# Performance work log

Measured on AMD Instinct MI355X. Metric: run time of the kernel, lower is better.

## Reference

```python
import jax, jax.numpy as jnp
import numpy as np

NUM_HEADS = 16


def setup_inputs() -> dict:
    key = jax.random.key(0)
    ks = jax.random.split(key, 8)
    B, N, C = 2, 1024, 1024
    H, D = NUM_HEADS, C // NUM_HEADS
    Npast = 8192
    s = 0.02
    return {
        "x": jax.random.normal(ks[0], (B, N, C), jnp.float32),
        "past_k": jax.random.normal(ks[1], (B, H, Npast, D), jnp.float32),
        "past_v": jax.random.normal(ks[2], (B, H, Npast, D), jnp.float32),
        "qkv_w": jax.random.normal(ks[3], (3 * C, C), jnp.float32) * s,
        "qkv_b": jax.random.normal(ks[4], (3 * C,), jnp.float32) * s,
        "proj_w": jax.random.normal(ks[5], (C, C), jnp.float32) * s,
        "proj_b": jax.random.normal(ks[6], (C,), jnp.float32) * s,
        "cache_budget": 4096,
    }


def reference(x, past_k, past_v, qkv_w, qkv_b, proj_w, proj_b, cache_budget):
    B, N, C = x.shape
    H = NUM_HEADS
    D = C // H
    scale = D ** -0.5

    # fused QKV projection -> [3, B, H, N, D]
    qkv = (x @ qkv_w.T + qkv_b).reshape(B, N, 3, H, D).transpose(2, 0, 3, 1, 4)
    q, k, v = qkv[0], qkv[1], qkv[2]

    # use_cache path: anchor tokens = current-frame token count on first call
    num_anchor = N
    k = jnp.concatenate([past_k, k], axis=2)  # [B,H,Ntot,D]
    v = jnp.concatenate([past_v, v], axis=2)
    Ntot = k.shape[2]

    # eviction: mean cosine-similarity scoring over candidate (non-anchor) keys.
    # mean_j cos(k_i, k_j) == khat_i . mean_j(khat_j) -- O(N*D), no NxN matrix.
    num_keep = cache_budget - num_anchor
    cand_k = k[:, :, num_anchor:, :]  # [B,H,Ncand,D]
    khat = cand_k / (jnp.linalg.norm(cand_k, axis=-1, keepdims=True) + 1e-6)
    mean_dir = khat.mean(axis=2, keepdims=True)
    mean_scores = (khat * mean_dir).sum(-1)  # [B,H,Ncand]
    # keep the least-redundant tokens (lowest mean similarity)
    _, top_idx = jax.lax.top_k(-mean_scores, num_keep)  # [B,H,num_keep]
    top_idx = jnp.sort(top_idx, axis=-1)
    avg_scores = mean_scores.mean()

    anchor_idx = jnp.broadcast_to(jnp.arange(num_anchor)[None, None, :], (B, H, num_anchor))
    keep_idx = jnp.concatenate([anchor_idx, top_idx + num_anchor], axis=2)  # [B,H,budget]
    gidx = keep_idx[..., None]
    k_new = jnp.take_along_axis(k, jnp.broadcast_to(gidx, (B, H, cache_budget, D)), axis=2)
    v_new = jnp.take_along_axis(v, jnp.broadcast_to(gidx, (B, H, cache_budget, D)), axis=2)

    # SDPA
    logits = jnp.einsum("bhqd,bhkd->bhqk", q, k_new) * scale
    attn = jax.nn.softmax(logits, axis=-1)
    o = jnp.einsum("bhqk,bhkd->bhqd", attn, v_new)
    o = o.transpose(0, 2, 1, 3).reshape(B, N, C)
    out = o @ proj_w.T + proj_b
    return out, k_new, v_new, avg_scores
```

## Files before the change

### kernel.cpp

```cpp
#include <hip/hip_runtime.h>
#include <hip/hip_bf16.h>
#include <math.h>

#define BB 2
#define HH 16
#define NN 1024
#define CC 1024
#define DD 64
#define NPAST 8192
#define NANCH 1024
#define CBUD 4096
#define NKEEP 3072
#define NCAND 8192
#define BH 32

#define TILEB 16384

#define OUT_SZ   (BB*NN*CC)
#define KNEW_OFF ((size_t)OUT_SZ)
#define KNEW_SZ  ((size_t)BH*CBUD*DD)
#define VNEW_OFF (KNEW_OFF + KNEW_SZ)
#define AVG_OFF  (VNEW_OFF + KNEW_SZ)

#define WS_KF   ((size_t)0)
#define WS_VF   ((size_t)2097152)
#define WS_VTS  ((size_t)0)
#define WS_XT   ((size_t)4194304)
#define WS_OT   ((size_t)4194304)
#define WS_WQVT ((size_t)5242880)
#define WS_WPT  ((size_t)5242880)
#define WS_QB   ((size_t)6291456)
#define WS_MD   ((size_t)7340032)
#define WS_SC   ((size_t)7342080)
#define WS_BS   ((size_t)7604224)
#define WS_SEL  ((size_t)7604288)
#define WS_MDP  ((size_t)7702592)
#define WS_BSP  ((size_t)7718976)

typedef __attribute__((ext_vector_type(8))) short short8;
typedef __attribute__((ext_vector_type(4))) float f32x4;

typedef unsigned int __attribute__((address_space(3))) lds_uint;
typedef unsigned int __attribute__((address_space(1))) glb_uint;

__device__ __forceinline__ void gload16(const void* g, void* l) {
    __builtin_amdgcn_global_load_lds((const glb_uint*)g, (lds_uint*)l, 16, 0, 0);
}

__device__ inline unsigned short f2bf(float f) {
    unsigned u = __float_as_uint(f);
    unsigned r = (u + 0x7FFFu + ((u >> 16) & 1u)) >> 16;
    return (unsigned short)r;
}
__device__ inline unsigned cvtpk(float a, float b) {
    __hip_bfloat162 h = __float22bfloat162_rn(make_float2(a, b));
    return *reinterpret_cast<unsigned*>(&h);
}
__device__ __forceinline__ float fexp2(float x) {
#if __has_builtin(__builtin_amdgcn_exp2f)
    return __builtin_amdgcn_exp2f(x);
#else
    return exp2f(x);
#endif
}

__global__ __launch_bounds__(256) void conv_xw(const float* __restrict__ x,
                                               const float* __restrict__ qw,
                                               unsigned short* __restrict__ xt,
                                               unsigned short* __restrict__ wqvt)
{
    int bid = blockIdx.x;
    int gid = (bid & 1023) * 256 + threadIdx.x;
    int r = gid >> 7, k0 = (gid & 127) * 8;
    const float* src;
    unsigned short* dst;
    int srow;
    if (bid < 1024) { src = x;  dst = xt;   srow = r; }
    else            { src = qw; dst = wqvt; srow = (r < 1024) ? r : r + 1024; }
    float4 a = *(const float4*)&src[(size_t)srow * 1024 + k0];
    float4 b = *(const float4*)&src[(size_t)srow * 1024 + k0 + 4];
    uint4 u;
    u.x = cvtpk(a.x, a.y); u.y = cvtpk(a.z, a.w);
    u.z = cvtpk(b.x, b.y); u.w = cvtpk(b.z, b.w);
    size_t tile = (size_t)(r >> 7) * 16 + (k0 >> 6);
    int inner = (((r & 127) * 128 + (k0 & 63) * 2)) ^ ((r & 7) << 4);
    *(uint4*)((char*)dst + tile * TILEB + inner) = u;
}

__global__ __launch_bounds__(256) void kf_gemm(const float* __restrict__ x,
                                               const float* __restrict__ w,
                                               const float* __restrict__ bias,
                                               float* __restrict__ ws)
{
    __shared__ float As[2][16][68];
    __shared__ float Bs[2][16][68];
    int tid = threadIdx.x;
    int m0 = blockIdx.y * 64;
    int n0 = blockIdx.x * 64;
    int tx = tid & 15, ty = tid >> 4;
    int lr = tid >> 2;
    int lk = (tid & 3) * 4;
    float acc[4][4] = {{0.f}};

    {
        float4 a = *(const float4*)&x[(size_t)(m0 + lr) * CC + lk];
        float4 b = *(const float4*)&w[(size_t)(1024 + n0 + lr) * CC + lk];
        As[0][lk+0][lr] = a.x; As[0][lk+1][lr] = a.y; As[0][lk+2][lr] = a.z; As[0][lk+3][lr] = a.w;
        Bs[0][lk+0][lr] = b.x; Bs[0][lk+1][lr] = b.y; Bs[0][lk+2][lr] = b.z; Bs[0][lk+3][lr] = b.w;
    }
    __syncthreads();

    int cur = 0;
    for (int k0 = 0; k0 < CC; k0 += 16) {
        float4 a, b;
        bool more = (k0 + 16 < CC);
        if (more) {
            a = *(const float4*)&x[(size_t)(m0 + lr) * CC + k0 + 16 + lk];
            b = *(const float4*)&w[(size_t)(1024 + n0 + lr) * CC + k0 + 16 + lk];
        }
        float tacc[4][4] = {{0.f}};
        #pragma unroll
        for (int kk = 0; kk < 16; ++kk) {
            float4 a4 = *(const float4*)&As[cur][kk][ty*4];
            float4 b4 = *(const float4*)&Bs[cur][kk][tx*4];
            float av[4] = {a4.x, a4.y, a4.z, a4.w};
            float bv[4] = {b4.x, b4.y, b4.z, b4.w};
            #pragma unroll
            for (int i = 0; i < 4; ++i)
                #pragma unroll
                for (int j = 0; j < 4; ++j)
                    tacc[i][j] += av[i] * bv[j];
        }
        #pragma unroll
        for (int i = 0; i < 4; ++i)
            #pragma unroll
            for (int j = 0; j < 4; ++j)
                acc[i][j] += tacc[i][j];
        if (more) {
            As[cur^1][lk+0][lr] = a.x; As[cur^1][lk+1][lr] = a.y;
            As[cur^1][lk+2][lr] = a.z; As[cur^1][lk+3][lr] = a.w;
            Bs[cur^1][lk+0][lr] = b.x; Bs[cur^1][lk+1][lr] = b.y;
            Bs[cur^1][lk+2][lr] = b.z; Bs[cur^1][lk+3][lr] = b.w;
        }
        __syncthreads();
        cur ^= 1;
    }

    int cn0 = n0 + tx * 4;
    int h = cn0 >> 6, dd0 = cn0 & 63;
    float4 b4 = *(const float4*)&bias[1024 + cn0];
    float* kf = ws + WS_KF;
    #pragma unroll
    for (int i = 0; i < 4; ++i) {
        int m = m0 + ty * 4 + i;
        int b2 = m >> 10, n = m & 1023;
        float4 t;
        t.x = acc[i][0] + b4.x; t.y = acc[i][1] + b4.y;
        t.z = acc[i][2] + b4.z; t.w = acc[i][3] + b4.w;
        *(float4*)&kf[(((size_t)b2*HH + h)*NN + n)*DD + dd0] = t;
    }
}

template<int MODE>
__global__ __launch_bounds__(256) void mfma_gemm(const unsigned short* __restrict__ At,
                                                 const unsigned short* __restrict__ Bt,
                                                 const float* __restrict__ bias,
                                                 float* __restrict__ outp)
{
    __shared__ char lds[131072];
    int tid = threadIdx.x;
    int w = tid >> 6, lane = tid & 63;
    int g = lane >> 4, r16 = lane & 15;
    int wr = w >> 1, wc = w & 1;
    int bm = blockIdx.y, bn = blockIdx.x;
    const int KB = 16;
    const float QSCL = 0.125f * 1.44269504089f;

    f32x4 acc[4][4];
    #pragma unroll
    for (int i = 0; i < 4; ++i)
        #pragma unroll
        for (int j = 0; j < 4; ++j) acc[i][j] = 0.f;

    const char* Abase = (const char*)At + (size_t)bm * KB * TILEB;
    const char* Bbase = (const char*)Bt + (size_t)bn * KB * TILEB;

    #pragma unroll
    for (int i = 0; i < 4; ++i) {
        gload16(Abase + (size_t)w*4096 + i*1024 + lane*16, lds + w*4096 + i*1024);
        gload16(Bbase + (size_t)w*4096 + i*1024 + lane*16, lds + TILEB + w*4096 + i*1024);
    }
    asm volatile("s_waitcnt vmcnt(0)" ::: "memory");
    __syncthreads();

    int cur = 0;
    for (int kb = 0; kb < KB; ++kb) {
        char* Acur = lds + cur * (2*TILEB);
        char* Bcur = Acur + TILEB;
        if (kb + 1 < KB) {
            char* Anxt = lds + (cur ^ 1) * (2*TILEB);
            char* Bnxt = Anxt + TILEB;
            const char* an = Abase + (size_t)(kb+1)*TILEB + w*4096;
            const char* bsrc = Bbase + (size_t)(kb+1)*TILEB + w*4096;
            #pragma unroll
            for (int i = 0; i < 4; ++i) {
                gload16(an + i*1024 + lane*16, Anxt + w*4096 + i*1024);
                gload16(bsrc + i*1024 + lane*16, Bnxt + w*4096 + i*1024);
            }
        }
        short8 a0[4], a1[4], b0[4], b1[4];
        #pragma unroll
        for (int mi = 0; mi < 4; ++mi) {
            int row = wr*64 + mi*16 + r16;
            int sw = (row & 7) << 4;
            a0[mi] = *(const short8*)(Acur + ((row*128 + g*16) ^ sw));
            a1[mi] = *(const short8*)(Acur + ((row*128 + 64 + g*16) ^ sw));
        }
        #pragma unroll
        for (int ni = 0; ni < 4; ++ni) {
            int row = wc*64 + ni*16 + r16;
            int sw = (row & 7) << 4;
            b0[ni] = *(const short8*)(Bcur + ((row*128 + g*16) ^ sw));
            b1[ni] = *(const short8*)(Bcur + ((row*128 + 64 + g*16) ^ sw));
        }
        __builtin_amdgcn_s_setprio(1);
        #pragma unroll
        for (int mi = 0; mi < 4; ++mi)
            #pragma unroll
            for (int ni = 0; ni < 4; ++ni) {
                acc[mi][ni] = __builtin_amdgcn_mfma_f32_16x16x32_bf16(a0[mi], b0[ni], acc[mi][ni], 0, 0, 0);
                acc[mi][ni] = __builtin_amdgcn_mfma_f32_16x16x32_bf16(a1[mi], b1[ni], acc[mi][ni], 0, 0, 0);
            }
        __builtin_amdgcn_s_setprio(0);
        asm volatile("s_waitcnt vmcnt(0)" ::: "memory");
        __syncthreads();
        cur ^= 1;
    }

    int nq = bn*128 + wc*64;
    float bv[4];
    #pragma unroll
    for (int ni = 0; ni < 4; ++ni) {
        int n = nq + ni*16 + r16;
        bv[ni] = (MODE == 0) ? bias[(n < 1024) ? n : (n + 1024)] : bias[n];
    }
    #pragma unroll
    for (int mi = 0; mi < 4; ++mi) {
        #pragma unroll
        for (int rr = 0; rr < 4; ++rr) {
            int ml = wr*64 + mi*16 + 4*g + rr;
            int mg = bm*128 + ml;
            int bb = mg >> 10, tok = mg & 1023;
            #pragma unroll
            for (int ni = 0; ni < 4; ++ni) {
                int n = nq + ni*16 + r16;
                float v = acc[mi][ni][rr] + bv[ni];
                if (MODE == 0) {
                    if (n < 1024) {
                        unsigned short* qb = (unsigned short*)(outp + WS_QB);
                        int hh = n >> 6, d = n & 63;
                        qb[(((size_t)bb*16 + hh)*1024 + tok)*64 + d] = f2bf(v * QSCL);
                    } else {
                        float* vf = outp + WS_VF;
                        int hh = (n - 1024) >> 6, d = n & 63;
                        vf[(((size_t)bb*16 + hh)*1024 + tok)*64 + d] = v;
                    }
                } else {
                    outp[(size_t)mg*1024 + n] = v;
                }
            }
        }
    }
}

__global__ __launch_bounds__(256) void meandir_part(const float* __restrict__ past_k,
                                                    float* __restrict__ ws)
{
    int bh = blockIdx.x, seg = blockIdx.y, tid = threadIdx.x;
    const float* kpast = past_k + (size_t)bh * NPAST * DD;
    const float* knew  = ws + WS_KF + (size_t)bh * NN * DD;
    float dir[64];
    #pragma unroll
    for (int i = 0; i < 64; ++i) dir[i] = 0.f;

    int j0 = seg * 1024;
    for (int jj = tid; jj < 1024; jj += 256) {
        int pos = NANCH + j0 + jj;
        const float* row = (pos < NPAST) ? (kpast + (size_t)pos * DD)
                                         : (knew + (size_t)(pos - NPAST) * DD);
        float v[64]; float ss = 0.f;
        #pragma unroll
        for (int g = 0; g < 16; ++g) {
            float4 t = *(const float4*)&row[g*4];
            v[4*g]=t.x; v[4*g+1]=t.y; v[4*g+2]=t.z; v[4*g+3]=t.w;
            ss += t.x*t.x + t.y*t.y + t.z*t.z + t.w*t.w;
        }
        float inv = 1.0f / (sqrtf(ss) + 1e-6f);
        #pragma unroll
        for (int i = 0; i < 64; ++i) dir[i] += v[i] * inv;
    }
    #pragma unroll
    for (int i = 0; i < 64; ++i)
        for (int off = 32; off; off >>= 1) dir[i] += __shfl_xor(dir[i], off);

    __shared__ float sdir[4][64];
    int lane = tid & 63, wid = tid >> 6;
    if (lane == 0) {
        #pragma unroll
        for (int i = 0; i < 64; ++i) sdir[wid][i] = dir[i];
    }
    __syncthreads();
    if (tid < 64) {
        float s = sdir[0][tid] + sdir[1][tid] + sdir[2][tid] + sdir[3][tid];
        ws[WS_MDP + ((size_t)bh*8 + seg)*DD + tid] = s;
    }
}

__global__ void meandir_red(float* __restrict__ ws)
{
    int bh = blockIdx.x, tid = threadIdx.x;
    float s = 0.f;
    #pragma unroll
    for (int seg = 0; seg < 8; ++seg)
        s += ws[WS_MDP + ((size_t)bh*8 + seg)*DD + tid];
    ws[WS_MD + (size_t)bh*DD + tid] = s * (1.0f / (float)NCAND);
}

__global__ __launch_bounds__(256) void scores_part(const float* __restrict__ past_k,
                                                   float* __restrict__ ws)
{
    __shared__ float md[64];
    __shared__ float sred[4];
    int bh = blockIdx.x, seg = blockIdx.y, tid = threadIdx.x;
    if (tid < 64) md[tid] = ws[WS_MD + (size_t)bh*DD + tid];
    __syncthreads();
    const float* kpast = past_k + (size_t)bh * NPAST * DD;
    const float* knew  = ws + WS_KF + (size_t)bh * NN * DD;
    float ssum = 0.f;
    int j0 = seg * 1024;
    for (int jj = tid; jj < 1024; jj += 256) {
        int j = j0 + jj;
        int pos = NANCH + j;
        const float* row = (pos < NPAST) ? (kpast + (size_t)pos * DD)
                                         : (knew + (size_t)(pos - NPAST) * DD);
        float ss = 0.f, dp = 0.f;
        #pragma unroll
        for (int g = 0; g < 16; ++g) {
            float4 t = *(const float4*)&row[g*4];
            ss += t.x*t.x + t.y*t.y + t.z*t.z + t.w*t.w;
            dp += t.x*md[4*g] + t.y*md[4*g+1] + t.z*md[4*g+2] + t.w*md[4*g+3];
        }
        float sc = dp / (sqrtf(ss) + 1e-6f);
        ws[WS_SC + (size_t)bh*NCAND + j] = sc;
        ssum += sc;
    }
    for (int off = 32; off; off >>= 1) ssum += __shfl_xor(ssum, off);
    int lane = tid & 63, wid = tid >> 6;
    if (lane == 0) sred[wid] = ssum;
    __syncthreads();
    if (tid == 0)
        ws[WS_BSP + (size_t)bh*8 + seg] = sred[0] + sred[1] + sred[2] + sred[3];
}

__global__ __launch_bounds__(1024) void topk_k(float* __restrict__ ws, int* __restrict__ sel,
                                               float* __restrict__ dout)
{
    __shared__ unsigned keys[NCAND];
    __shared__ int hist[256];
    __shared__ int red[16];
    __shared__ int red2[16];
    __shared__ float fred[16];
    __shared__ int bcast;
    __shared__ unsigned bbyte;
    int bh = blockIdx.x, tid = threadIdx.x;
    int lane = tid & 63, wid = tid >> 6;

    if (bh == 0) {
        float v = (tid < 256) ? ws[WS_BSP + tid] : 0.f;
        for (int off = 32; off; off >>= 1) v += __shfl_xor(v, off);
        if (lane == 0) fred[wid] = v;
        __syncthreads();
        if (tid == 0) {
            float s = 0.f;
            for (int i = 0; i < 16; ++i) s += fred[i];
            dout[AVG_OFF] = s * (1.0f / ((float)BH * (float)NCAND));
        }
        __syncthreads();
    }

    for (int j = tid; j < NCAND; j += 1024) {
        unsigned u = __float_as_uint(ws[WS_SC + (size_t)bh*NCAND + j]);
        u ^= (u & 0x80000000u) ? 0xFFFFFFFFu : 0x80000000u;
        keys[j] = u;
    }
    __syncthreads();

    int rem = NKEEP;
    unsigned prefix = 0;
    #pragma unroll
    for (int pass = 0; pass < 4; ++pass) {
        int shift = 24 - 8*pass;
        if (tid < 256) hist[tid] = 0;
        __syncthreads();
        unsigned himask = (pass == 0) ? 0u : (0xFFFFFFFFu << (shift + 8));
        for (int j = tid; j < NCAND; j += 1024) {
            unsigned k = keys[j];
            if ((k & himask) == prefix)
                atomicAdd(&hist[(k >> shift) & 255], 1);
        }
        __syncthreads();
        if (tid == 0) {
            int cum = 0, b = 0;
            for (; b < 255; ++b) {
                if (rem <= cum + hist[b]) break;
                cum += hist[b];
            }
            bcast = cum;
            bbyte = (unsigned)b;
        }
        __syncthreads();
        rem -= bcast;
        prefix |= (bbyte << shift);
        __syncthreads();
    }
    unsigned T = prefix;

    {
        int cnt = 0;
        for (int j = tid; j < NCAND; j += 1024) cnt += (int)(keys[j] < T);
        for (int off = 32; off; off >>= 1) cnt += __shfl_xor(cnt, off);
        if (lane == 0) red[wid] = cnt;
        __syncthreads();
        if (tid == 0) { int c = 0; for (int i = 0; i < 16; ++i) c += red[i]; bcast = c; }
        __syncthreads();
    }
    int c_less = bcast;
    int ttie = NKEEP - c_less;

    int base = tid * 8;
    unsigned kv[8]; int lcnt = 0, ecnt = 0;
    #pragma unroll
    for (int i = 0; i < 8; ++i) {
        kv[i] = keys[base + i];
        lcnt += (int)(kv[i] < T);
        ecnt += (int)(kv[i] == T);
    }
    int li = lcnt, ei = ecnt;
    for (int off = 1; off < 64; off <<= 1) {
        int tl = __shfl_up(li, off);
        int te = __shfl_up(ei, off);
        if (lane >= off) { li += tl; ei += te; }
    }
    __syncthreads();
    if (lane == 63) { red[wid] = li; red2[wid] = ei; }
    __syncthreads();
    int lb = 0, eb = 0;
    for (int w = 0; w < wid; ++w) { lb += red[w]; eb += red2[w]; }
    lb += li - lcnt; eb += ei - ecnt;
    #pragma unroll
    for (int i = 0; i < 8; ++i) {
        bool less = kv[i] < T, eq = kv[i] == T;
        if (less || (eq && eb < ttie)) {
            int pos = lb + (eb < ttie ? eb : ttie);
            sel[(size_t)bh*NKEEP + pos] = base + i;
        }
        lb += (int)less; eb += (int)eq;
    }
}

__global__ __launch_bounds__(256) void gather_k(const float* __restrict__ past_k,
                                                const float* __restrict__ past_v,
                                                const float* __restrict__ ws,
                                                const int* __restrict__ sel,
                                                float* __restrict__ dout)
{
    int gid = blockIdx.x * 256 + threadIdx.x;
    int row = gid >> 4, lane = gid & 15;
    int bh = row >> 12, r = row & 4095;
    int pos = (r < NANCH) ? r : (NANCH + sel[(size_t)bh*NKEEP + (r - NANCH)]);
    const float *kr, *vr;
    if (pos < NPAST) {
        kr = past_k + ((size_t)bh*NPAST + pos) * DD;
        vr = past_v + ((size_t)bh*NPAST + pos) * DD;
    } else {
        kr = ws + WS_KF + ((size_t)bh*NN + (pos - NPAST)) * DD;
        vr = ws + WS_VF + ((size_t)bh*NN + (pos - NPAST)) * DD;
    }
    float4 kq = *(const float4*)&kr[lane*4];
    float4 vq = *(const float4*)&vr[lane*4];
    *(float4*)&dout[KNEW_OFF + ((size_t)bh*CBUD + r)*DD + lane*4] = kq;
    *(float4*)&dout[VNEW_OFF + ((size_t)bh*CBUD + r)*DD + lane*4] = vq;
}

__global__ __launch_bounds__(256) void vtrans_conv(const float* __restrict__ dout,
                                                   unsigned short* __restrict__ vt,
                                                   const float* __restrict__ pw,
                                                   unsigned short* __restrict__ wpt)
{
    if (blockIdx.x >= 2048) {
        int gid = (blockIdx.x - 2048) * 256 + threadIdx.x;
        int r = gid >> 7, k0 = (gid & 127) * 8;
        float4 a = *(const float4*)&pw[(size_t)r * 1024 + k0];
        float4 b = *(const float4*)&pw[(size_t)r * 1024 + k0 + 4];
        uint4 u;
        u.x = cvtpk(a.x, a.y); u.y = cvtpk(a.z, a.w);
        u.z = cvtpk(b.x, b.y); u.w = cvtpk(b.z, b.w);
        size_t tile = (size_t)(r >> 7) * 16 + (k0 >> 6);
        int inner = (((r & 127) * 128 + (k0 & 63) * 2)) ^ ((r & 7) << 4);
        *(uint4*)((char*)wpt + tile * TILEB + inner) = u;
        return;
    }
    __shared__ unsigned short S[64][65];
    int bh = blockIdx.x >> 6, kt = blockIdx.x & 63;
    int c0 = kt * 64;
    int tid = threadIdx.x;
    int r = tid >> 2, c4 = (tid & 3) * 16;
    const float* src = dout + VNEW_OFF + ((size_t)bh*CBUD + c0 + r)*DD + c4;
    #pragma unroll
    for (int i = 0; i < 4; ++i) {
        float4 f = *(const float4*)&src[i*4];
        S[r][c4 + i*4 + 0] = f2bf(f.x);
        S[r][c4 + i*4 + 1] = f2bf(f.y);
        S[r][c4 + i*4 + 2] = f2bf(f.z);
        S[r][c4 + i*4 + 3] = f2bf(f.w);
    }
    __syncthreads();
    int d = r, k4 = c4;
    uint4 u0, u1;
    u0.x = (unsigned)S[k4+0][d] | ((unsigned)S[k4+1][d] << 16);
    u0.y = (unsigned)S[k4+2][d] | ((unsigned)S[k4+3][d] << 16);
    u0.z = (unsigned)S[k4+4][d] | ((unsigned)S[k4+5][d] << 16);
    u0.w = (unsigned)S[k4+6][d] | ((unsigned)S[k4+7][d] << 16);
    u1.x = (unsigned)S[k4+8][d] | ((unsigned)S[k4+9][d] << 16);
    u1.y = (unsigned)S[k4+10][d] | ((unsigned)S[k4+11][d] << 16);
    u1.z = (unsigned)S[k4+12][d] | ((unsigned)S[k4+13][d] << 16);
    u1.w = (unsigned)S[k4+14][d] | ((unsigned)S[k4+15][d] << 16);
    size_t tbase = ((size_t)bh*64 + kt) * 8192;
    int sw = (d & 7) << 4;
    *(uint4*)((char*)vt + tbase + ((d*128 + k4*2)      ^ sw)) = u0;
    *(uint4*)((char*)vt + tbase + ((d*128 + k4*2 + 16) ^ sw)) = u1;
}

__global__ __launch_bounds__(256) void attn_mfma(const unsigned short* __restrict__ qb,
                                                 const float* __restrict__ dout,
                                                 const unsigned short* __restrict__ vt,
                                                 unsigned short* __restrict__ ot)
{
    __shared__ char kls[2][2][8192];
    __shared__ char vls[2][2][8192];
    __shared__ char pls[4][2048];

    int orig = blockIdx.x;
    int bid = (orig & 7) * 64 + (orig >> 3);
    int bh = bid >> 4, qt = bid & 15;
    int b = bh >> 4, h = bh & 15;
    int tid = threadIdx.x;
    int w = tid >> 6, lane = tid & 63;
    int g = lane >> 4, r16 = lane & 15;
    int q0 = qt * 64 + w * 16;

    const unsigned short* qrow = qb + ((size_t)bh*NN + q0 + r16) * DD;
    short8 qa0 = *(const short8*)&qrow[8*g];
    short8 qa1 = *(const short8*)&qrow[32 + 8*g];

    const float* kf = dout + KNEW_OFF + (size_t)bh * CBUD * DD;
    const char* vtt = (const char*)vt + (size_t)bh * 64 * 8192;
    char* plw = pls[w];
    int psw = (r16 & 7) << 4;

    int srA = tid >> 3;
    int srB = srA + 32;
    int scb = (tid & 7) * 16;
    int d0  = scb >> 1;
    int sdA = (srA*128 + scb) ^ ((srA & 7) << 4);
    int sdB = (srB*128 + scb) ^ ((srB & 7) << 4);

    f32x4 accd[4];
    #pragma unroll
    for (int dt = 0; dt < 4; ++dt) accd[dt] = 0.f;
    float lsum = 0.f;

    {
        gload16(vtt + tid*16,               vls[0][0] + tid*16);
        gload16(vtt + 4096 + tid*16,        vls[0][0] + 4096 + tid*16);
        gload16(vtt + 8192 + tid*16,        vls[0][1] + tid*16);
        gload16(vtt + 8192 + 4096 + tid*16, vls[0][1] + 4096 + tid*16);
        #pragma unroll
        for (int hh = 0; hh < 2; ++hh) {
            const float* ksA = kf + ((size_t)hh*64 + srA) * DD + d0;
            const float* ksB = kf + ((size_t)hh*64 + srB) * DD + d0;
            float4 a0 = *(const float4*)ksA, a1 = *(const float4*)(ksA + 4);
            float4 b0 = *(const float4*)ksB, b1 = *(const float4*)(ksB + 4);
            uint4 kuA, kuB;
            kuA.x = cvtpk(a0.x,a0.y); kuA.y = cvtpk(a0.z,a0.w);
            kuA.z = cvtpk(a1.x,a1.y); kuA.w = cvtpk(a1.z,a1.w);
            kuB.x = cvtpk(b0.x,b0.y); kuB.y = cvtpk(b0.z,b0.w);
            kuB.z = cvtpk(b1.x,b1.y); kuB.w = cvtpk(b1.z,b1.w);
            *(uint4*)&kls[0][hh][sdA] = kuA;
            *(uint4*)&kls[0][hh][sdB] = kuB;
        }
    }
    __syncthreads();

    int cur = 0;
    for (int t = 0; t < 32; ++t) {
        float4 na0[2], na1[2], nb0[2], nb1[2];
        bool more = (t + 1 < 32);
        if (more) {
            int nt = 2*t + 2;
            gload16(vtt + (size_t)nt*8192 + tid*16,            vls[cur^1][0] + tid*16);
            gload16(vtt + (size_t)nt*8192 + 4096 + tid*16,     vls[cur^1][0] + 4096 + tid*16);
            gload16(vtt + (size_t)(nt+1)*8192 + tid*16,        vls[cur^1][1] + tid*16);
            gload16(vtt + (size_t)(nt+1)*8192 + 4096 + tid*16, vls[cur^1][1] + 4096 + tid*16);
            #pragma unroll
            for (int hh = 0; hh < 2; ++hh) {
                const float* ksA = kf + ((size_t)(nt+hh)*64 + srA) * DD + d0;
                const float* ksB = kf + ((size_t)(nt+hh)*64 + srB) * DD + d0;
                na0[hh] = *(const float4*)ksA; na1[hh] = *(const float4*)(ksA + 4);
                nb0[hh] = *(const float4*)ksB; nb1[hh] = *(const float4*)(ksB + 4);
            }
        }

        #pragma unroll
        for (int hh = 0; hh < 2; ++hh) {
            const char* kb = kls[cur][hh];
            f32x4 sacc[4];
            #pragma unroll
            for (int t4 = 0; t4 < 4; ++t4) sacc[t4] = 0.f;
            __builtin_amdgcn_s_setprio(1);
            #pragma unroll
            for (int t4 = 0; t4 < 4; ++t4) {
                int row = 16*t4 + r16;
                int sw = (r16 & 7) << 4;
                short8 ka0 = *(const short8*)(kb + ((row*128 + g*16) ^ sw));
                short8 ka1 = *(const short8*)(kb + ((row*128 + 64 + g*16) ^ sw));
                sacc[t4] = __builtin_amdgcn_mfma_f32_16x16x32_bf16(ka0, qa0, sacc[t4], 0, 0, 0);
                sacc[t4] = __builtin_amdgcn_mfma_f32_16x16x32_bf16(ka1, qa1, sacc[t4], 0, 0, 0);
            }
            __builtin_amdgcn_s_setprio(0);

            float p[4][4];
            float ps = 0.f;
            #pragma unroll
            for (int t4 = 0; t4 < 4; ++t4) {
                p[t4][0] = fexp2(sacc[t4][0]);
                p[t4][1] = fexp2(sacc[t4][1]);
                p[t4][2] = fexp2(sacc[t4][2]);
                p[t4][3] = fexp2(sacc[t4][3]);
                ps += (p[t4][0] + p[t4][1]) + (p[t4][2] + p[t4][3]);
            }
            lsum += ps;
            #pragma unroll
            for (int t4 = 0; t4 < 4; ++t4) {
                uint2 u;
                u.x = cvtpk(p[t4][0], p[t4][1]);
                u.y = cvtpk(p[t4][2], p[t4][3]);
                int cb = (16*t4 + 4*g) * 2;
                *(uint2*)&plw[(r16*128 + cb) ^ psw] = u;
            }

            short8 pa0 = *(const short8*)&plw[(r16*128 + 16*g)      ^ psw];
            short8 pa1 = *(const short8*)&plw[(r16*128 + 64 + 16*g) ^ psw];
            const char* vb = vls[cur][hh];
            __builtin_amdgcn_s_setprio(1);
            #pragma unroll
            for (int dt = 0; dt < 4; ++dt) {
                int row = dt*16 + r16;
                int sw = (r16 & 7) << 4;
                short8 vb0 = *(const short8*)(vb + ((row*128 + g*16) ^ sw));
                short8 vb1 = *(const short8*)(vb + ((row*128 + 64 + g*16) ^ sw));
                accd[dt] = __builtin_amdgcn_mfma_f32_16x16x32_bf16(pa0, vb0, accd[dt], 0, 0, 0);
                accd[dt] = __builtin_amdgcn_mfma_f32_16x16x32_bf16(pa1, vb1, accd[dt], 0, 0, 0);
            }
            __builtin_amdgcn_s_setprio(0);
        }

        if (more) {
            #pragma unroll
            for (int hh = 0; hh < 2; ++hh) {
                uint4 kuA, kuB;
                kuA.x = cvtpk(na0[hh].x, na0[hh].y); kuA.y = cvtpk(na0[hh].z, na0[hh].w);
                kuA.z = cvtpk(na1[hh].x, na1[hh].y); kuA.w = cvtpk(na1[hh].z, na1[hh].w);
                kuB.x = cvtpk(nb0[hh].x, nb0[hh].y); kuB.y = cvtpk(nb0[hh].z, nb0[hh].w);
                kuB.z = cvtpk(nb1[hh].x, nb1[hh].y); kuB.w = cvtpk(nb1[hh].z, nb1[hh].w);
                *(uint4*)&kls[cur^1][hh][sdA] = kuA;
                *(uint4*)&kls[cur^1][hh][sdB] = kuB;
            }
        }
        __syncthreads();
        cur ^= 1;
    }

    lsum += __shfl_xor(lsum, 16);
    lsum += __shfl_xor(lsum, 32);
    float ivl = 1.0f / lsum;
    float iq[4];
    #pragma unroll
    for (int rr = 0; rr < 4; ++rr) iq[rr] = __shfl(ivl, 20*g + rr);
    #pragma unroll
    for (int dt = 0; dt < 4; ++dt) {
        #pragma unroll
        for (int rr = 0; rr < 4; ++rr) {
            int q = q0 + 4*g + rr;
            int mrow = b*1024 + q;
            int d = dt*16 + r16;
            size_t tile = (size_t)(mrow >> 7) * 16 + h;
            int inner = ((mrow & 127)*128 + d*2) ^ ((mrow & 7) << 4);
            *(unsigned short*)((char*)ot + tile*TILEB + inner) = f2bf(accd[dt][rr] * iq[rr]);
        }
    }
}

extern "C" void kernel_launch(void* const* d_in, const int* in_sizes, int n_in,
                              void* d_out, int out_size, void* d_ws, size_t ws_size,
                              hipStream_t stream)
{
    (void)in_sizes; (void)n_in; (void)out_size; (void)ws_size;
    const float* x      = (const float*)d_in[0];
    const float* past_k = (const float*)d_in[1];
    const float* past_v = (const float*)d_in[2];
    const float* qkv_w  = (const float*)d_in[3];
    const float* qkv_b  = (const float*)d_in[4];
    const float* proj_w = (const float*)d_in[5];
    const float* proj_b = (const float*)d_in[6];
    float* out = (float*)d_out;
    float* ws  = (float*)d_ws;
    int*   sel = (int*)(ws + WS_SEL);
    unsigned short* xt   = (unsigned short*)(ws + WS_XT);
    unsigned short* wqvt = (unsigned short*)(ws + WS_WQVT);
    unsigned short* wpt  = (unsigned short*)(ws + WS_WPT);
    unsigned short* qbp  = (unsigned short*)(ws + WS_QB);
    unsigned short* vtp  = (unsigned short*)(ws + WS_VTS);
    unsigned short* otp  = (unsigned short*)(ws + WS_OT);

    conv_xw<<<2048, 256, 0, stream>>>(x, qkv_w, xt, wqvt);
    kf_gemm<<<dim3(16, 32), 256, 0, stream>>>(x, qkv_w, qkv_b, ws);
    mfma_gemm<0><<<dim3(16, 16), 256, 0, stream>>>(xt, wqvt, qkv_b, ws);
    meandir_part<<<dim3(32, 8), 256, 0, stream>>>(past_k, ws);
    meandir_red<<<32, 64, 0, stream>>>(ws);
    scores_part<<<dim3(32, 8), 256, 0, stream>>>(past_k, ws);
    topk_k<<<32, 1024, 0, stream>>>(ws, sel, out);
    gather_k<<<8192, 256, 0, stream>>>(past_k, past_v, ws, sel, out);
    vtrans_conv<<<2560, 256, 0, stream>>>(out, vtp, proj_w, wpt);
    attn_mfma<<<512, 256, 0, stream>>>(qbp, out, vtp, otp);
    mfma_gemm<1><<<dim3(8, 16), 256, 0, stream>>>(otp, wpt, proj_b, out);
}
```

Measured before the change: 283.7 us.

## Pre-convert K_new to swizzled bf16 tiles and async-load them in attention

Adds a pre-pass in vtrans_conv that converts the gathered fp32 K cache into swizzled bf16 64x64 tiles in workspace, so the attention kernel can stream K with global_load_lds like V instead of loading fp32 and converting per block. It also doubles the k-step of the fp32 K-projection GEMM and hoists the LDS offset computations in the attention loop. The K path is used only when the workspace is large enough, and costs an extra global write and read of the bf16 K tiles.

```diff
diff --git a/kernel.cpp b/kernel.cpp
--- a/kernel.cpp
+++ b/kernel.cpp
@@ -36,6 +36,7 @@
 #define WS_SEL  ((size_t)7604288)
 #define WS_MDP  ((size_t)7702592)
 #define WS_BSP  ((size_t)7718976)
+#define WS_KTS  ((size_t)7719232)
 
 typedef __attribute__((ext_vector_type(8))) short short8;
 typedef __attribute__((ext_vector_type(4))) float f32x4;
@@ -92,8 +93,8 @@
                                                const float* __restrict__ bias,
                                                float* __restrict__ ws)
 {
-    __shared__ float As[2][16][68];
-    __shared__ float Bs[2][16][68];
+    __shared__ float As[2][32][68];
+    __shared__ float Bs[2][32][68];
     int tid = threadIdx.x;
     int m0 = blockIdx.y * 64;
     int n0 = blockIdx.x * 64;
@@ -103,44 +104,57 @@
     float acc[4][4] = {{0.f}};
 
     {
-        float4 a = *(const float4*)&x[(size_t)(m0 + lr) * CC + lk];
-        float4 b = *(const float4*)&w[(size_t)(1024 + n0 + lr) * CC + lk];
-        As[0][lk+0][lr] = a.x; As[0][lk+1][lr] = a.y; As[0][lk+2][lr] = a.z; As[0][lk+3][lr] = a.w;
-        Bs[0][lk+0][lr] = b.x; Bs[0][lk+1][lr] = b.y; Bs[0][lk+2][lr] = b.z; Bs[0][lk+3][lr] = b.w;
+        float4 a0 = *(const float4*)&x[(size_t)(m0 + lr) * CC + lk];
+        float4 a1 = *(const float4*)&x[(size_t)(m0 + lr) * CC + lk + 16];
+        float4 b0 = *(const float4*)&w[(size_t)(1024 + n0 + lr) * CC + lk];
+        float4 b1 = *(const float4*)&w[(size_t)(1024 + n0 + lr) * CC + lk + 16];
+        As[0][lk+0][lr] = a0.x; As[0][lk+1][lr] = a0.y; As[0][lk+2][lr] = a0.z; As[0][lk+3][lr] = a0.w;
+        As[0][lk+16][lr] = a1.x; As[0][lk+17][lr] = a1.y; As[0][lk+18][lr] = a1.z; As[0][lk+19][lr] = a1.w;
+        Bs[0][lk+0][lr] = b0.x; Bs[0][lk+1][lr] = b0.y; Bs[0][lk+2][lr] = b0.z; Bs[0][lk+3][lr] = b0.w;
+        Bs[0][lk+16][lr] = b1.x; Bs[0][lk+17][lr] = b1.y; Bs[0][lk+18][lr] = b1.z; Bs[0][lk+19][lr] = b1.w;
     }
     __syncthreads();
 
     int cur = 0;
-    for (int k0 = 0; k0 < CC; k0 += 16) {
-        float4 a, b;
-        bool more = (k0 + 16 < CC);
+    for (int k0 = 0; k0 < CC; k0 += 32) {
+        float4 a0, a1, b0, b1;
+        bool more = (k0 + 32 < CC);
         if (more) {
-            a = *(const float4*)&x[(size_t)(m0 + lr) * CC + k0 + 16 + lk];
-            b = *(const float4*)&w[(size_t)(1024 + n0 + lr) * CC + k0 + 16 + lk];
-        }
-        float tacc[4][4] = {{0.f}};
-        #pragma unroll
-        for (int kk = 0; kk < 16; ++kk) {
-            float4 a4 = *(const float4*)&As[cur][kk][ty*4];
-            float4 b4 = *(const float4*)&Bs[cur][kk][tx*4];
-            float av[4] = {a4.x, a4.y, a4.z, a4.w};
-            float bv[4] = {b4.x, b4.y, b4.z, b4.w};
+            a0 = *(const float4*)&x[(size_t)(m0 + lr) * CC + k0 + 32 + lk];
+            a1 = *(const float4*)&x[(size_t)(m0 + lr) * CC + k0 + 48 + lk];
+            b0 = *(const float4*)&w[(size_t)(1024 + n0 + lr) * CC + k0 + 32 + lk];
+            b1 = *(const float4*)&w[(size_t)(1024 + n0 + lr) * CC + k0 + 48 + lk];
+        }
+        #pragma unroll
+        for (int ch = 0; ch < 2; ++ch) {
+            float tacc[4][4] = {{0.f}};
+            #pragma unroll
+            for (int kk = 0; kk < 16; ++kk) {
+                float4 a4 = *(const float4*)&As[cur][ch*16 + kk][ty*4];
+                float4 b4 = *(const float4*)&Bs[cur][ch*16 + kk][tx*4];
+                float av[4] = {a4.x, a4.y, a4.z, a4.w};
+                float bv[4] = {b4.x, b4.y, b4.z, b4.w};
+                #pragma unroll
+                for (int i = 0; i < 4; ++i)
+                    #pragma unroll
+                    for (int j = 0; j < 4; ++j)
+                        tacc[i][j] += av[i] * bv[j];
+            }
             #pragma unroll
             for (int i = 0; i < 4; ++i)
                 #pragma unroll
                 for (int j = 0; j < 4; ++j)
-                    tacc[i][j] += av[i] * bv[j];
-        }
-        #pragma unroll
-        for (int i = 0; i < 4; ++i)
-            #pragma unroll
-            for (int j = 0; j < 4; ++j)
-                acc[i][j] += tacc[i][j];
+                    acc[i][j] += tacc[i][j];
+        }
         if (more) {
-            As[cur^1][lk+0][lr] = a.x; As[cur^1][lk+1][lr] = a.y;
-            As[cur^1][lk+2][lr] = a.z; As[cur^1][lk+3][lr] = a.w;
-            Bs[cur^1][lk+0][lr] = b.x; Bs[cur^1][lk+1][lr] = b.y;
-            Bs[cur^1][lk+2][lr] = b.z; Bs[cur^1][lk+3][lr] = b.w;
+            As[cur^1][lk+0][lr] = a0.x; As[cur^1][lk+1][lr] = a0.y;
+            As[cur^1][lk+2][lr] = a0.z; As[cur^1][lk+3][lr] = a0.w;
+            As[cur^1][lk+16][lr] = a1.x; As[cur^1][lk+17][lr] = a1.y;
+            As[cur^1][lk+18][lr] = a1.z; As[cur^1][lk+19][lr] = a1.w;
+            Bs[cur^1][lk+0][lr] = b0.x; Bs[cur^1][lk+1][lr] = b0.y;
+            Bs[cur^1][lk+2][lr] = b0.z; Bs[cur^1][lk+3][lr] = b0.w;
+            Bs[cur^1][lk+16][lr] = b1.x; Bs[cur^1][lk+17][lr] = b1.y;
+            Bs[cur^1][lk+18][lr] = b1.z; Bs[cur^1][lk+19][lr] = b1.w;
         }
         __syncthreads();
         cur ^= 1;
@@ -495,10 +509,34 @@
 __global__ __launch_bounds__(256) void vtrans_conv(const float* __restrict__ dout,
                                                    unsigned short* __restrict__ vt,
                                                    const float* __restrict__ pw,
-                                                   unsigned short* __restrict__ wpt)
-{
-    if (blockIdx.x >= 2048) {
-        int gid = (blockIdx.x - 2048) * 256 + threadIdx.x;
+                                                   unsigned short* __restrict__ wpt,
+                                                   unsigned short* __restrict__ ktp,
+                                                   int nkblk)
+{
+    int bid = blockIdx.x;
+    if (bid >= 2048 && bid < 2048 + nkblk) {
+        int bid2 = bid - 2048;
+        int bh = bid2 >> 6, kt = bid2 & 63;
+        int tid = threadIdx.x;
+        int r = tid >> 2, c4 = (tid & 3) * 16;
+        const float* kn = dout + KNEW_OFF + ((size_t)bh*CBUD + kt*64 + r)*DD + c4;
+        float4 f0 = *(const float4*)&kn[0];
+        float4 f1 = *(const float4*)&kn[4];
+        float4 f2 = *(const float4*)&kn[8];
+        float4 f3 = *(const float4*)&kn[12];
+        uint4 u0, u1;
+        u0.x = cvtpk(f0.x,f0.y); u0.y = cvtpk(f0.z,f0.w);
+        u0.z = cvtpk(f1.x,f1.y); u0.w = cvtpk(f1.z,f1.w);
+        u1.x = cvtpk(f2.x,f2.y); u1.y = cvtpk(f2.z,f2.w);
+        u1.z = cvtpk(f3.x,f3.y); u1.w = cvtpk(f3.z,f3.w);
+        size_t tbase = ((size_t)bh*64 + kt) * 8192;
+        int sw = (r & 7) << 4;
+        *(uint4*)((char*)ktp + tbase + ((r*128 + c4*2)      ^ sw)) = u0;
+        *(uint4*)((char*)ktp + tbase + ((r*128 + c4*2 + 16) ^ sw)) = u1;
+        return;
+    }
+    if (bid >= 2048 + nkblk) {
+        int gid = (bid - 2048 - nkblk) * 256 + threadIdx.x;
         int r = gid >> 7, k0 = (gid & 127) * 8;
         float4 a = *(const float4*)&pw[(size_t)r * 1024 + k0];
         float4 b = *(const float4*)&pw[(size_t)r * 1024 + k0 + 4];
@@ -511,7 +549,7 @@
         return;
     }
     __shared__ unsigned short S[64][65];
-    int bh = blockIdx.x >> 6, kt = blockIdx.x & 63;
+    int bh = bid >> 6, kt = bid & 63;
     int c0 = kt * 64;
     int tid = threadIdx.x;
     int r = tid >> 2, c4 = (tid & 3) * 16;
@@ -541,9 +579,11 @@
     *(uint4*)((char*)vt + tbase + ((d*128 + k4*2 + 16) ^ sw)) = u1;
 }
 
+template<int KTS>
 __global__ __launch_bounds__(256) void attn_mfma(const unsigned short* __restrict__ qb,
                                                  const float* __restrict__ dout,
                                                  const unsigned short* __restrict__ vt,
+                                                 const unsigned short* __restrict__ ktp,
                                                  unsigned short* __restrict__ ot)
 {
     __shared__ char kls[2][2][8192];
@@ -565,11 +605,25 @@
 
     const float* kf = dout + KNEW_OFF + (size_t)bh * CBUD * DD;
     const char* vtt = (const char*)vt + (size_t)bh * 64 * 8192;
+    const char* ktt = (const char*)ktp + (size_t)bh * 64 * 8192;
     char* plw = pls[w];
     int psw = (r16 & 7) << 4;
 
-    int srA = tid >> 3;
-    int srB = srA + 32;
+    int ro[8];
+    #pragma unroll
+    for (int t4 = 0; t4 < 4; ++t4) {
+        int row = 16*t4 + r16;
+        ro[2*t4]   = (row*128 + g*16) ^ psw;
+        ro[2*t4+1] = (row*128 + 64 + g*16) ^ psw;
+    }
+    int pwo[4];
+    #pragma unroll
+    for (int t4 = 0; t4 < 4; ++t4)
+        pwo[t4] = (r16*128 + (16*t4 + 4*g)*2) ^ psw;
+    int pro0 = (r16*128 + 16*g) ^ psw;
+    int pro1 = (r16*128 + 64 + 16*g) ^ psw;
+
+    int srA = tid >> 3, srB = srA + 32;
     int scb = (tid & 7) * 16;
     int d0  = scb >> 1;
     int sdA = (srA*128 + scb) ^ ((srA & 7) << 4);
@@ -581,23 +635,30 @@
     float lsum = 0.f;
 
     {
-        gload16(vtt + tid*16,               vls[0][0] + tid*16);
-        gload16(vtt + 4096 + tid*16,        vls[0][0] + 4096 + tid*16);
-        gload16(vtt + 8192 + tid*16,        vls[0][1] + tid*16);
-        gload16(vtt + 8192 + 4096 + tid*16, vls[0][1] + 4096 + tid*16);
-        #pragma unroll
-        for (int hh = 0; hh < 2; ++hh) {
-            const float* ksA = kf + ((size_t)hh*64 + srA) * DD + d0;
-            const float* ksB = kf + ((size_t)hh*64 + srB) * DD + d0;
-            float4 a0 = *(const float4*)ksA, a1 = *(const float4*)(ksA + 4);
-            float4 b0 = *(const float4*)ksB, b1 = *(const float4*)(ksB + 4);
-            uint4 kuA, kuB;
-            kuA.x = cvtpk(a0.x,a0.y); kuA.y = cvtpk(a0.z,a0.w);
-            kuA.z = cvtpk(a1.x,a1.y); kuA.w = cvtpk(a1.z,a1.w);
-            kuB.x = cvtpk(b0.x,b0.y); kuB.y = cvtpk(b0.z,b0.w);
-            kuB.z = cvtpk(b1.x,b1.y); kuB.w = cvtpk(b1.z,b1.w);
-            *(uint4*)&kls[0][hh][sdA] = kuA;
-            *(uint4*)&kls[0][hh][sdB] = kuB;
+        gload16(vtt + tid*16,         vls[0][0] + tid*16);
+        gload16(vtt + 4096 + tid*16,  vls[0][0] + 4096 + tid*16);
+        gload16(vtt + 8192 + tid*16,  vls[0][1] + tid*16);
+        gload16(vtt + 12288 + tid*16, vls[0][1] + 4096 + tid*16);
+        if (KTS) {
+            gload16(ktt + tid*16,         kls[0][0] + tid*16);
+            gload16(ktt + 4096 + tid*16,  kls[0][0] + 4096 + tid*16);
+            gload16(ktt + 8192 + tid*16,  kls[0][1] + tid*16);
+            gload16(ktt + 12288 + tid*16, kls[0][1] + 4096 + tid*16);
+        } else {
+            #pragma unroll
+            for (int hh = 0; hh < 2; ++hh) {
+                const float* ksA = kf + ((size_t)hh*64 + srA) * DD + d0;
+                const float* ksB = kf + ((size_t)hh*64 + srB) * DD + d0;
+                float4 a0 = *(const float4*)ksA, a1 = *(const float4*)(ksA + 4);
+                float4 b0 = *(const float4*)ksB, b1 = *(const float4*)(ksB + 4);
+                uint4 kuA, kuB;
+                kuA.x = cvtpk(a0.x,a0.y); kuA.y = cvtpk(a0.z,a0.w);
+                kuA.z = cvtpk(a1.x,a1.y); kuA.w = cvtpk(a1.z,a1.w);
+                kuB.x = cvtpk(b0.x,b0.y); kuB.y = cvtpk(b0.z,b0.w);
+                kuB.z = cvtpk(b1.x,b1.y); kuB.w = cvtpk(b1.z,b1.w);
+                *(uint4*)&kls[0][hh][sdA] = kuA;
+                *(uint4*)&kls[0][hh][sdB] = kuB;
+            }
         }
     }
     __syncthreads();
@@ -608,16 +669,25 @@
         bool more = (t + 1 < 32);
         if (more) {
             int nt = 2*t + 2;
-            gload16(vtt + (size_t)nt*8192 + tid*16,            vls[cur^1][0] + tid*16);
-            gload16(vtt + (size_t)nt*8192 + 4096 + tid*16,     vls[cur^1][0] + 4096 + tid*16);
-            gload16(vtt + (size_t)(nt+1)*8192 + tid*16,        vls[cur^1][1] + tid*16);
-            gload16(vtt + (size_t)(nt+1)*8192 + 4096 + tid*16, vls[cur^1][1] + 4096 + tid*16);
-            #pragma unroll
-            for (int hh = 0; hh < 2; ++hh) {
-                const float* ksA = kf + ((size_t)(nt+hh)*64 + srA) * DD + d0;
-                const float* ksB = kf + ((size_t)(nt+hh)*64 + srB) * DD + d0;
-                na0[hh] = *(const float4*)ksA; na1[hh] = *(const float4*)(ksA + 4);
-                nb0[hh] = *(const float4*)ksB; nb1[hh] = *(const float4*)(ksB + 4);
+            const char* vsrc = vtt + (size_t)nt*8192;
+            gload16(vsrc + tid*16,         vls[cur^1][0] + tid*16);
+            gload16(vsrc + 4096 + tid*16,  vls[cur^1][0] + 4096 + tid*16);
+            gload16(vsrc + 8192 + tid*16,  vls[cur^1][1] + tid*16);
+            gload16(vsrc + 12288 + tid*16, vls[cur^1][1] + 4096 + tid*16);
+            if (KTS) {
+                const char* ksrc = ktt + (size_t)nt*8192;
+                gload16(ksrc + tid*16,         kls[cur^1][0] + tid*16);
+                gload16(ksrc + 4096 + tid*16,  kls[cur^1][0] + 4096 + tid*16);
+                gload16(ksrc + 8192 + tid*16,  kls[cur^1][1] + tid*16);
+                gload16(ksrc + 12288 + tid*16, kls[cur^1][1] + 4096 + tid*16);
+            } else {
+                #pragma unroll
+                for (int hh = 0; hh < 2; ++hh) {
+                    const float* ksA = kf + ((size_t)(nt+hh)*64 + srA) * DD + d0;
+                    const float* ksB = kf + ((size_t)(nt+hh)*64 + srB) * DD + d0;
+                    na0[hh] = *(const float4*)ksA; na1[hh] = *(const float4*)(ksA + 4);
+                    nb0[hh] = *(const float4*)ksB; nb1[hh] = *(const float4*)(ksB + 4);
+                }
             }
         }
 
@@ -630,10 +700,8 @@
             __builtin_amdgcn_s_setprio(1);
             #pragma unroll
             for (int t4 = 0; t4 < 4; ++t4) {
-                int row = 16*t4 + r16;
-                int sw = (r16 & 7) << 4;
-                short8 ka0 = *(const short8*)(kb + ((row*128 + g*16) ^ sw));
-                short8 ka1 = *(const short8*)(kb + ((row*128 + 64 + g*16) ^ sw));
+                short8 ka0 = *(const short8*)(kb + ro[2*t4]);
+                short8 ka1 = *(const short8*)(kb + ro[2*t4+1]);
                 sacc[t4] = __builtin_amdgcn_mfma_f32_16x16x32_bf16(ka0, qa0, sacc[t4], 0, 0, 0);
                 sacc[t4] = __builtin_amdgcn_mfma_f32_16x16x32_bf16(ka1, qa1, sacc[t4], 0, 0, 0);
             }
@@ -655,27 +723,24 @@
                 uint2 u;
                 u.x = cvtpk(p[t4][0], p[t4][1]);
                 u.y = cvtpk(p[t4][2], p[t4][3]);
-                int cb = (16*t4 + 4*g) * 2;
-                *(uint2*)&plw[(r16*128 + cb) ^ psw] = u;
-            }
-
-            short8 pa0 = *(const short8*)&plw[(r16*128 + 16*g)      ^ psw];
-            short8 pa1 = *(const short8*)&plw[(r16*128 + 64 + 16*g) ^ psw];
+                *(uint2*)&plw[pwo[t4]] = u;
+            }
+
+            short8 pa0 = *(const short8*)&plw[pro0];
+            short8 pa1 = *(const short8*)&plw[pro1];
             const char* vb = vls[cur][hh];
             __builtin_amdgcn_s_setprio(1);
             #pragma unroll
             for (int dt = 0; dt < 4; ++dt) {
-                int row = dt*16 + r16;
-                int sw = (r16 & 7) << 4;
-                short8 vb0 = *(const short8*)(vb + ((row*128 + g*16) ^ sw));
-                short8 vb1 = *(const short8*)(vb + ((row*128 + 64 + g*16) ^ sw));
+                short8 vb0 = *(const short8*)(vb + ro[2*dt]);
+                short8 vb1 = *(const short8*)(vb + ro[2*dt+1]);
                 accd[dt] = __builtin_amdgcn_mfma_f32_16x16x32_bf16(pa0, vb0, accd[dt], 0, 0, 0);
                 accd[dt] = __builtin_amdgcn_mfma_f32_16x16x32_bf16(pa1, vb1, accd[dt], 0, 0, 0);
             }
             __builtin_amdgcn_s_setprio(0);
         }
 
-        if (more) {
+        if (more && !KTS) {
             #pragma unroll
             for (int hh = 0; hh < 2; ++hh) {
                 uint4 kuA, kuB;
@@ -715,7 +780,7 @@
                               void* d_out, int out_size, void* d_ws, size_t ws_size,
                               hipStream_t stream)
 {
-    (void)in_sizes; (void)n_in; (void)out_size; (void)ws_size;
+    (void)in_sizes; (void)n_in; (void)out_size;
     const float* x      = (const float*)d_in[0];
     const float* past_k = (const float*)d_in[1];
     const float* past_v = (const float*)d_in[2];
@@ -732,6 +797,10 @@
     unsigned short* qbp  = (unsigned short*)(ws + WS_QB);
     unsigned short* vtp  = (unsigned short*)(ws + WS_VTS);
     unsigned short* otp  = (unsigned short*)(ws + WS_OT);
+    unsigned short* ktp  = (unsigned short*)(ws + WS_KTS);
+
+    int use_kts = (ws_size >= (size_t)(WS_KTS + 4194304) * sizeof(float)) ? 1 : 0;
+    int nkblk = use_kts ? 2048 : 0;
 
     conv_xw<<<2048, 256, 0, stream>>>(x, qkv_w, xt, wqvt);
     kf_gemm<<<dim3(16, 32), 256, 0, stream>>>(x, qkv_w, qkv_b, ws);
@@ -741,7 +810,10 @@
     scores_part<<<dim3(32, 8), 256, 0, stream>>>(past_k, ws);
     topk_k<<<32, 1024, 0, stream>>>(ws, sel, out);
     gather_k<<<8192, 256, 0, stream>>>(past_k, past_v, ws, sel, out);
-    vtrans_conv<<<2560, 256, 0, stream>>>(out, vtp, proj_w, wpt);
-    attn_mfma<<<512, 256, 0, stream>>>(qbp, out, vtp, otp);
+    vtrans_conv<<<2048 + nkblk + 512, 256, 0, stream>>>(out, vtp, proj_w, wpt, ktp, nkblk);
+    if (use_kts)
+        attn_mfma<1><<<512, 256, 0, stream>>>(qbp, out, vtp, ktp, otp);
+    else
+        attn_mfma<0><<<512, 256, 0, stream>>>(qbp, out, vtp, ktp, otp);
     mfma_gemm<1><<<dim3(8, 16), 256, 0, stream>>>(otp, wpt, proj_b, out);
 }
```

Result: slower. 310.5 us (+9.5%).
